# Optimization experiments

Hardware: AMD Instinct MI355X
Metric: run time of the kernel (lower is better)

The kernel has to match this reference:

```python
import math
import jax, jax.numpy as jnp
import numpy as np

D = 4  # BWGNN d


def calculate_theta2(d):
    # Faithful numeric reimplementation of the sympy version.
    # f_i(x) = (x/2)^i (1-x/2)^(d-i) / (2*Beta(i+1, d+1-i)); the original code
    # keeps only the d lowest-order (ascending) coefficients, dropping x^d.
    thetas = []
    for i in range(d):
        c1 = np.zeros(i + 1); c1[i] = 0.5 ** i                      # (x/2)^i
        c2 = np.array([math.comb(d - i, j) * (-0.5) ** j
                       for j in range(d - i + 1)])                   # (1-x/2)^(d-i)
        c = np.convolve(c1, c2)                                      # ascending, len d+1
        B = math.factorial(i) * math.factorial(d - i) / math.factorial(d + 1)
        c = c / (2.0 * B)
        thetas.append([float(c[j]) for j in range(d)])               # coeff[d-i] slicing
    return thetas

THETAS = calculate_theta2(D)


def setup_inputs() -> dict:
    key = jax.random.key(0)
    k1, k2, k3, k4 = jax.random.split(key, 4)
    N, E, F_in, H = 100000, 1600000, 128, 64
    feature = jax.random.normal(k1, (N, F_in), dtype=jnp.float32)
    edge_index = jax.random.randint(k2, (2, E), 0, N, dtype=jnp.int32)
    W = jax.random.normal(k3, (F_in, H), dtype=jnp.float32) * 0.05
    b = jax.random.normal(k4, (H,), dtype=jnp.float32) * 0.05
    return {"feature": feature, "edge_index": edge_index, "W": W, "b": b}


def reference(feature, edge_index, W, b):
    N = feature.shape[0]
    src, dst = edge_index[0], edge_index[1]
    # out_degrees: number of out-edges per node (src side), clamped to >= 1
    deg = jax.ops.segment_sum(jnp.ones_like(src, dtype=jnp.float32), src,
                              num_segments=N)
    D_invsqrt = jnp.maximum(deg, 1.0) ** -0.5  # [N]
    D_invsqrt = D_invsqrt[:, None]             # [N,1]

    h = jax.nn.leaky_relu(feature @ W + b, negative_slope=0.01)  # [N,H]

    def unn_laplacian(feat):
        # feat - D^{-1/2} A^T D^{-1/2} feat  (copy_u + sum over dst)
        msg = (feat * D_invsqrt)[src]                          # [E,H]
        agg = jax.ops.segment_sum(msg, dst, num_segments=N)    # [N,H]
        return feat - agg * D_invsqrt

    outs = []
    for theta in THETAS:
        feat = h
        acc = theta[0] * feat
        for k in range(1, len(theta)):
            feat = unn_laplacian(feat)
            acc = acc + theta[k] * feat
        outs.append(acc)
    return jnp.concatenate(outs, axis=1)  # [N, len(THETAS)*H]
```

## Files before the change

### kernel.cpp

```cpp
#include <hip/hip_runtime.h>

#define THREADS 256
#define T1 4096
#define BCAP 8192
#define NBMAX 512

__device__ __forceinline__ float bf2f(unsigned short u) {
    return __uint_as_float(((unsigned int)u) << 16);
}
__device__ __forceinline__ unsigned short f2bf(float x) {
    unsigned int u = __float_as_uint(x);
    u += 0x7fffu + ((u >> 16) & 1u);
    return (unsigned short)(u >> 16);
}

__global__ void zero_kernel(int* __restrict__ p, int n) {
    const int i = blockIdx.x * blockDim.x + threadIdx.x;
    if (i < n) p[i] = 0;
}

__global__ void bin_kernel(const int* __restrict__ key, const int* __restrict__ val,
                           int* __restrict__ gFill, unsigned int* __restrict__ gBuf, int E) {
    __shared__ int cnt[NBMAX], scanB[NBMAX], gbase[NBMAX], place[NBMAX];
    __shared__ unsigned int stage[T1];
    __shared__ unsigned int stageAddr[T1];
    const int tid = threadIdx.x;
    const int tileStart = blockIdx.x * T1;
    const int tileCnt = min(T1, E - tileStart);

    for (int i = tid; i < NBMAX; i += THREADS) { cnt[i] = 0; place[i] = 0; }
    __syncthreads();

    for (int i = tid; i < tileCnt; i += THREADS)
        atomicAdd(&cnt[key[tileStart + i] >> 8], 1);
    __syncthreads();

    if (tid < 64) {
        const int base = tid * 8;
        int loc[8]; int s = 0;
        #pragma unroll
        for (int k = 0; k < 8; ++k) { loc[k] = s; s += cnt[base + k]; }
        int run = s;
        #pragma unroll
        for (int off = 1; off < 64; off <<= 1) {
            int t = __shfl_up(run, off);
            if (tid >= off) run += t;
        }
        const int excl = run - s;
        #pragma unroll
        for (int k = 0; k < 8; ++k) scanB[base + k] = excl + loc[k];
    }
    __syncthreads();

    for (int i = tid; i < NBMAX; i += THREADS)
        gbase[i] = atomicAdd(&gFill[i], cnt[i]);
    __syncthreads();

    for (int i = tid; i < tileCnt; i += THREADS) {
        const int kk = key[tileStart + i];
        const int vv = val[tileStart + i];
        const int b = kk >> 8;
        const unsigned int rec = ((unsigned int)(kk & 255) << 17) | (unsigned int)vv;
        const int pos = atomicAdd(&place[b], 1);
        const int li = scanB[b] + pos;
        const int gi = gbase[b] + pos;
        stage[li] = rec;
        stageAddr[li] = (gi < BCAP) ? (unsigned int)(b * BCAP + gi) : 0xFFFFFFFFu;
    }
    __syncthreads();

    for (int i = tid; i < tileCnt; i += THREADS) {
        const unsigned int a = stageAddr[i];
        if (a != 0xFFFFFFFFu) gBuf[a] = stage[i];
    }
}

__global__ void scanb_kernel(const int* __restrict__ gFill, int* __restrict__ gBase,
                             int* __restrict__ rowptr, int nb, int N) {
    __shared__ int s[NBMAX];
    const int tid = threadIdx.x;
    const int v = (tid < nb) ? min(gFill[tid], BCAP) : 0;
    s[tid] = v;
    __syncthreads();
    for (int off = 1; off < NBMAX; off <<= 1) {
        int t = (tid >= off) ? s[tid - off] : 0;
        __syncthreads();
        s[tid] += t;
        __syncthreads();
    }
    if (tid < nb) gBase[tid] = s[tid] - v;
    if (tid == NBMAX - 1) rowptr[N] = s[NBMAX - 1];
}

__global__ void csr_kernel(const int* __restrict__ gFill, const int* __restrict__ gBase,
                           const unsigned int* __restrict__ gBuf,
                           int* __restrict__ rowptr, int* __restrict__ col, int N) {
    __shared__ int fillT[256], offT[256], place[256], sc[256];
    __shared__ int colT[BCAP];
    __shared__ int nwrite;
    const int tid = threadIdx.x;
    const int b = blockIdx.x;
    const int nrec = min(gFill[b], BCAP);
    const int base = gBase[b];

    fillT[tid] = 0; place[tid] = 0;
    __syncthreads();
    for (int i = tid; i < nrec; i += THREADS)
        atomicAdd(&fillT[gBuf[(size_t)b * BCAP + i] >> 17], 1);
    __syncthreads();

    int v = fillT[tid];
    sc[tid] = v;
    __syncthreads();
    for (int off = 1; off < 256; off <<= 1) {
        int t = (tid >= off) ? sc[tid - off] : 0;
        __syncthreads();
        sc[tid] += t;
        __syncthreads();
    }
    offT[tid] = sc[tid] - v;
    if (tid == 255) nwrite = sc[255];
    __syncthreads();

    const int node0 = b << 8;
    const int nvalid = min(256, N - node0);
    if (tid < nvalid) rowptr[node0 + tid] = base + offT[tid];

    for (int i = tid; i < nrec; i += THREADS) {
        const unsigned int rec = gBuf[(size_t)b * BCAP + i];
        const int dlow = rec >> 17;
        const int s = rec & 0x1FFFF;
        const int pos = atomicAdd(&place[dlow], 1);
        colT[offT[dlow] + pos] = s;
    }
    __syncthreads();

    const int nw = nwrite;
    for (int i = tid; i < nw; i += THREADS) col[base + i] = colT[i];
}

__global__ void deg_kernel2(const int* __restrict__ gFill, const unsigned int* __restrict__ gBuf,
                            int* __restrict__ deg, int N) {
    __shared__ int cntT[256];
    const int tid = threadIdx.x;
    const int b = blockIdx.x;
    const int nrec = min(gFill[b], BCAP);
    for (int i = tid; i < 256; i += THREADS) cntT[i] = 0;
    __syncthreads();
    for (int i = tid; i < nrec; i += THREADS)
        atomicAdd(&cntT[gBuf[(size_t)b * BCAP + i] >> 17], 1);
    __syncthreads();
    const int node0 = b << 8;
    const int nvalid = min(256, N - node0);
    for (int t = tid; t < nvalid; t += THREADS) deg[node0 + t] = cntT[t];
}

__global__ void count_fb(const int* __restrict__ src, const int* __restrict__ dst,
                         int* __restrict__ deg, int* __restrict__ cntd, int E) {
    const int stride = gridDim.x * blockDim.x;
    for (int i = blockIdx.x * blockDim.x + threadIdx.x; i < E; i += stride) {
        atomicAdd(&deg[src[i]], 1);
        atomicAdd(&cntd[dst[i]], 1);
    }
}
__global__ void scan_fb(const int* __restrict__ cnt, int* __restrict__ rowptr, int N) {
    __shared__ int s[256];
    __shared__ int carry;
    const int tid = threadIdx.x;
    if (tid == 0) carry = 0;
    __syncthreads();
    for (int basei = 0; basei < N; basei += 256) {
        const int i = basei + tid;
        const int v = (i < N) ? cnt[i] : 0;
        s[tid] = v;
        __syncthreads();
        for (int off = 1; off < 256; off <<= 1) {
            int t = (tid >= off) ? s[tid - off] : 0;
            __syncthreads();
            s[tid] += t;
            __syncthreads();
        }
        if (i < N) rowptr[i] = carry + s[tid] - v;
        __syncthreads();
        if (tid == 0) carry += s[255];
        __syncthreads();
    }
    if (tid == 0) rowptr[N] = carry;
}
__global__ void fill_fb(const int* __restrict__ src, const int* __restrict__ dst,
                        const int* __restrict__ rowptr, int* __restrict__ place,
                        int* __restrict__ col, int E) {
    const int stride = gridDim.x * blockDim.x;
    for (int i = blockIdx.x * blockDim.x + threadIdx.x; i < E; i += stride) {
        const int d = dst[i];
        col[rowptr[d] + atomicAdd(&place[d], 1)] = src[i];
    }
}

__global__ void gemm_leaky(const float* __restrict__ feat, const float* __restrict__ W,
                           const float* __restrict__ b, const int* __restrict__ deg,
                           float* __restrict__ out, int N) {
    __shared__ float Wl[128 * 64];
    __shared__ float fl[64][132];
    __shared__ float bl[64];

    {
        const float4* W4 = (const float4*)W;
        float4* Wl4 = (float4*)Wl;
        for (int i = threadIdx.x; i < 2048; i += THREADS) Wl4[i] = W4[i];
        if (threadIdx.x < 64) bl[threadIdx.x] = b[threadIdx.x];
    }

    const int cg = threadIdx.x & 15;
    const int rg = threadIdx.x >> 4;
    const int ntiles = (N + 63) >> 6;
    char* base = (char*)out;

    for (int tile = blockIdx.x; tile < ntiles; tile += gridDim.x) {
        const int n0 = tile << 6;
        __syncthreads();
        for (int i = threadIdx.x; i < 2048; i += THREADS) {
            int rr = i >> 5;
            int kk = i & 31;
            float4 v = make_float4(0.f, 0.f, 0.f, 0.f);
            if (n0 + rr < N) v = ((const float4*)(feat + (size_t)(n0 + rr) * 128))[kk];
            *((float4*)&fl[rr][kk * 4]) = v;
        }
        __syncthreads();

        float acc[4][4];
        #pragma unroll
        for (int j = 0; j < 4; ++j) {
            float bv = bl[cg * 4 + j];
            acc[0][j] = bv; acc[1][j] = bv; acc[2][j] = bv; acc[3][j] = bv;
        }

        #pragma unroll 4
        for (int k = 0; k < 128; ++k) {
            const float4 w = *((const float4*)&Wl[k * 64 + cg * 4]);
            const float f0 = fl[rg * 4 + 0][k];
            const float f1 = fl[rg * 4 + 1][k];
            const float f2 = fl[rg * 4 + 2][k];
            const float f3 = fl[rg * 4 + 3][k];
            acc[0][0] += f0 * w.x; acc[0][1] += f0 * w.y; acc[0][2] += f0 * w.z; acc[0][3] += f0 * w.w;
            acc[1][0] += f1 * w.x; acc[1][1] += f1 * w.y; acc[1][2] += f1 * w.z; acc[1][3] += f1 * w.w;
            acc[2][0] += f2 * w.x; acc[2][1] += f2 * w.y; acc[2][2] += f2 * w.z; acc[2][3] += f2 * w.w;
            acc[3][0] += f3 * w.x; acc[3][1] += f3 * w.y; acc[3][2] += f3 * w.z; acc[3][3] += f3 * w.w;
        }

        #pragma unroll
        for (int i = 0; i < 4; ++i) {
            const int n = n0 + rg * 4 + i;
            if (n < N) {
                const float dv = rsqrtf(fmaxf((float)deg[n], 1.0f));
                ushort4 o;
                float v0 = acc[i][0] > 0.f ? acc[i][0] : 0.01f * acc[i][0];
                float v1 = acc[i][1] > 0.f ? acc[i][1] : 0.01f * acc[i][1];
                float v2 = acc[i][2] > 0.f ? acc[i][2] : 0.01f * acc[i][2];
                float v3 = acc[i][3] > 0.f ? acc[i][3] : 0.01f * acc[i][3];
                o.x = f2bf(v0 * dv); o.y = f2bf(v1 * dv); o.z = f2bf(v2 * dv); o.w = f2bf(v3 * dv);
                *((ushort4*)(base + (size_t)n * 1024 + cg * 8)) = o;
            }
        }
    }
}

__global__ void hop_kernel(const int* __restrict__ rowptr, const int* __restrict__ col,
                           const int* __restrict__ deg, float* __restrict__ out,
                           int N, int prevOff, int nextOff) {
    const int lane = threadIdx.x & 63;
    const int nwaves = (gridDim.x * blockDim.x) >> 6;
    char* base = (char*)out;
    for (int n = (blockIdx.x * blockDim.x + threadIdx.x) >> 6; n < N; n += nwaves) {
        const int beg = rowptr[n];
        const int end = rowptr[n + 1];
        float acc = 0.0f;
        for (int e0 = beg; e0 < end; e0 += 64) {
            const int idx = e0 + lane;
            const int c = (idx < end) ? col[idx] : 0;
            const int m = min(64, end - e0);
            int j = 0;
            for (; j + 4 <= m; j += 4) {
                const int s0 = __shfl(c, j);
                const int s1 = __shfl(c, j + 1);
                const int s2 = __shfl(c, j + 2);
                const int s3 = __shfl(c, j + 3);
                const float v0 = bf2f(*(const unsigned short*)(base + (size_t)s0 * 1024 + prevOff + lane * 2));
                const float v1 = bf2f(*(const unsigned short*)(base + (size_t)s1 * 1024 + prevOff + lane * 2));
                const float v2 = bf2f(*(const unsigned short*)(base + (size_t)s2 * 1024 + prevOff + lane * 2));
                const float v3 = bf2f(*(const unsigned short*)(base + (size_t)s3 * 1024 + prevOff + lane * 2));
                acc += (v0 + v1) + (v2 + v3);
            }
            for (; j < m; ++j) {
                const int s = __shfl(c, j);
                acc += bf2f(*(const unsigned short*)(base + (size_t)s * 1024 + prevOff + lane * 2));
            }
        }
        const float own = bf2f(*(const unsigned short*)(base + (size_t)n * 1024 + prevOff + lane * 2));
        const float d = fmaxf((float)deg[n], 1.0f);
        const float sn = own - acc / d;
        *(unsigned short*)(base + (size_t)n * 1024 + nextOff + lane * 2) = f2bf(sn);
    }
}

__global__ void combine_kernel(float* __restrict__ out, const int* __restrict__ deg, int N) {
    const int lane = threadIdx.x & 63;
    const int nwaves = (gridDim.x * blockDim.x) >> 6;
    char* base = (char*)out;
    for (int n = (blockIdx.x * blockDim.x + threadIdx.x) >> 6; n < N; n += nwaves) {
        char* row = base + (size_t)n * 1024;
        const float s0 = bf2f(*(const unsigned short*)(row + 0   + lane * 2));
        const float s1 = bf2f(*(const unsigned short*)(row + 128 + lane * 2));
        const float s2 = bf2f(*(const unsigned short*)(row + 256 + lane * 2));
        const float s3 = bf2f(*(const unsigned short*)(row + 384 + lane * 2));
        const float sc = sqrtf(fmaxf((float)deg[n], 1.0f));
        const float h  = s0 * sc;
        const float p1 = s1 * sc;
        const float p2 = s2 * sc;
        const float p3 = s3 * sc;
        const float o0 = 2.5f * h - 5.0f * p1 + 3.75f * p2 - 1.25f * p3;
        const float o1 = 5.0f * p1 - 7.5f * p2 + 3.75f * p3;
        const float o2 = 3.75f * (p2 - p3);
        const float o3 = 1.25f * p3;
        float* frow = (float*)row;
        frow[lane]       = o0;
        frow[64 + lane]  = o1;
        frow[128 + lane] = o2;
        frow[192 + lane] = o3;
    }
}

extern "C" void kernel_launch(void* const* d_in, const int* in_sizes, int n_in,
                              void* d_out, int out_size, void* d_ws, size_t ws_size,
                              hipStream_t stream) {
    const float* feature = (const float*)d_in[0];
    const int*   eidx    = (const int*)d_in[1];
    const float* W       = (const float*)d_in[2];
    const float* b       = (const float*)d_in[3];
    float* out = (float*)d_out;

    const int N = in_sizes[0] / 128;
    const int E = in_sizes[1] / 2;
    const int* src = eidx;
    const int* dst = eidx + E;

    const int nb = (N + 255) >> 8;

    int* deg    = (int*)d_ws;
    int* fill   = deg + N;
    int* rowptr = fill + N;
    int* col    = rowptr + (N + 1);
    int* gFillD = col + E;
    int* gFillS = gFillD + NBMAX;
    int* gBase  = gFillS + NBMAX;
    unsigned int* gBufD = (unsigned int*)(gBase + NBMAX);
    unsigned int* gBufS = gBufD + (size_t)nb * BCAP;

    if (N <= 131072) {
        zero_kernel<<<(2 * NBMAX + THREADS - 1) / THREADS, THREADS, 0, stream>>>(gFillD, 2 * NBMAX);
        const int tiles = (E + T1 - 1) / T1;
        bin_kernel<<<tiles, THREADS, 0, stream>>>(dst, src, gFillD, gBufD, E);
        bin_kernel<<<tiles, THREADS, 0, stream>>>(src, src, gFillS, gBufS, E);
        scanb_kernel<<<1, NBMAX, 0, stream>>>(gFillD, gBase, rowptr, nb, N);
        csr_kernel<<<nb, THREADS, 0, stream>>>(gFillD, gBase, gBufD, rowptr, col, N);
        deg_kernel2<<<nb, THREADS, 0, stream>>>(gFillS, gBufS, deg, N);
    } else {
        zero_kernel<<<(2 * N + THREADS - 1) / THREADS, THREADS, 0, stream>>>(deg, 2 * N);
        count_fb<<<2048, THREADS, 0, stream>>>(src, dst, deg, fill, E);
        scan_fb<<<1, 256, 0, stream>>>(fill, rowptr, N);
        zero_kernel<<<(N + THREADS - 1) / THREADS, THREADS, 0, stream>>>(fill, N);
        fill_fb<<<2048, THREADS, 0, stream>>>(src, dst, rowptr, fill, col, E);
    }

    const int gemm_blocks = (N + 63) / 64;
    gemm_leaky<<<gemm_blocks, THREADS, 0, stream>>>(feature, W, b, deg, out, N);

    const int gblocks = (N + 3) / 4;
    hop_kernel<<<gblocks, THREADS, 0, stream>>>(rowptr, col, deg, out, N, 0, 128);
    hop_kernel<<<gblocks, THREADS, 0, stream>>>(rowptr, col, deg, out, N, 128, 256);
    hop_kernel<<<gblocks, THREADS, 0, stream>>>(rowptr, col, deg, out, N, 256, 384);

    combine_kernel<<<gblocks, THREADS, 0, stream>>>(out, deg, N);
}
```

Measured before the change: 288.4 us.

## Use compact bf16 hop buffers, fuse combine into last hop, merge binning passes

The per-hop bf16 states move out of the strided 1KB output rows into dense 128-byte-per-node workspace buffers. This improves cache-line use on the random neighbour gathers. The gather now has each 16-lane group load a ushort4 for a different edge, handling 4 edges per step, and reduces across groups with xor shuffles. The separate combine kernel is folded into the last hop, and the two edge-binning launches are merged into one kernel with a smaller tile so one edge read serves both. The cost is more workspace memory and extra shuffle reductions per node.

```diff
diff --git a/kernel.cpp b/kernel.cpp
--- a/kernel.cpp
+++ b/kernel.cpp
@@ -1,7 +1,7 @@
 #include <hip/hip_runtime.h>
 
 #define THREADS 256
-#define T1 4096
+#define T1 2048
 #define BCAP 8192
 #define NBMAX 512
 
@@ -19,24 +19,34 @@
     if (i < n) p[i] = 0;
 }
 
-__global__ void bin_kernel(const int* __restrict__ key, const int* __restrict__ val,
-                           int* __restrict__ gFill, unsigned int* __restrict__ gBuf, int E) {
-    __shared__ int cnt[NBMAX], scanB[NBMAX], gbase[NBMAX], place[NBMAX];
-    __shared__ unsigned int stage[T1];
-    __shared__ unsigned int stageAddr[T1];
+__global__ void bin2_kernel(const int* __restrict__ src, const int* __restrict__ dst,
+                            int* __restrict__ gFillD, unsigned int* __restrict__ gBufD,
+                            int* __restrict__ gFillS, unsigned int* __restrict__ gBufS, int E) {
+    __shared__ int cntD[NBMAX], scanD[NBMAX], gbaseD[NBMAX], placeD[NBMAX];
+    __shared__ int cntS[NBMAX], scanS[NBMAX], gbaseS[NBMAX], placeS[NBMAX];
+    __shared__ unsigned int stageD[T1], addrD[T1];
+    __shared__ unsigned int stageS[T1], addrS[T1];
     const int tid = threadIdx.x;
     const int tileStart = blockIdx.x * T1;
     const int tileCnt = min(T1, E - tileStart);
 
-    for (int i = tid; i < NBMAX; i += THREADS) { cnt[i] = 0; place[i] = 0; }
-    __syncthreads();
-
-    for (int i = tid; i < tileCnt; i += THREADS)
-        atomicAdd(&cnt[key[tileStart + i] >> 8], 1);
-    __syncthreads();
-
-    if (tid < 64) {
-        const int base = tid * 8;
+    for (int i = tid; i < NBMAX; i += THREADS) {
+        cntD[i] = 0; placeD[i] = 0; cntS[i] = 0; placeS[i] = 0;
+    }
+    __syncthreads();
+
+    for (int i = tid; i < tileCnt; i += THREADS) {
+        atomicAdd(&cntD[dst[tileStart + i] >> 8], 1);
+        atomicAdd(&cntS[src[tileStart + i] >> 8], 1);
+    }
+    __syncthreads();
+
+    if (tid < 128) {
+        const int w = tid >> 6;
+        const int l = tid & 63;
+        const int* cnt = w ? cntS : cntD;
+        int* sout = w ? scanS : scanD;
+        const int base = l * 8;
         int loc[8]; int s = 0;
         #pragma unroll
         for (int k = 0; k < 8; ++k) { loc[k] = s; s += cnt[base + k]; }
@@ -44,34 +54,48 @@
         #pragma unroll
         for (int off = 1; off < 64; off <<= 1) {
             int t = __shfl_up(run, off);
-            if (tid >= off) run += t;
+            if (l >= off) run += t;
         }
         const int excl = run - s;
         #pragma unroll
-        for (int k = 0; k < 8; ++k) scanB[base + k] = excl + loc[k];
-    }
-    __syncthreads();
-
-    for (int i = tid; i < NBMAX; i += THREADS)
-        gbase[i] = atomicAdd(&gFill[i], cnt[i]);
+        for (int k = 0; k < 8; ++k) sout[base + k] = excl + loc[k];
+    }
+    __syncthreads();
+
+    for (int i = tid; i < NBMAX; i += THREADS) {
+        gbaseD[i] = atomicAdd(&gFillD[i], cntD[i]);
+        gbaseS[i] = atomicAdd(&gFillS[i], cntS[i]);
+    }
     __syncthreads();
 
     for (int i = tid; i < tileCnt; i += THREADS) {
-        const int kk = key[tileStart + i];
-        const int vv = val[tileStart + i];
-        const int b = kk >> 8;
-        const unsigned int rec = ((unsigned int)(kk & 255) << 17) | (unsigned int)vv;
-        const int pos = atomicAdd(&place[b], 1);
-        const int li = scanB[b] + pos;
-        const int gi = gbase[b] + pos;
-        stage[li] = rec;
-        stageAddr[li] = (gi < BCAP) ? (unsigned int)(b * BCAP + gi) : 0xFFFFFFFFu;
+        const int ss = src[tileStart + i];
+        const int dd = dst[tileStart + i];
+        {
+            const int b = dd >> 8;
+            const unsigned int rec = ((unsigned int)(dd & 255) << 17) | (unsigned int)ss;
+            const int pos = atomicAdd(&placeD[b], 1);
+            const int li = scanD[b] + pos;
+            const int gi = gbaseD[b] + pos;
+            stageD[li] = rec;
+            addrD[li] = (gi < BCAP) ? (unsigned int)(b * BCAP + gi) : 0xFFFFFFFFu;
+        }
+        {
+            const int b = ss >> 8;
+            const int pos = atomicAdd(&placeS[b], 1);
+            const int li = scanS[b] + pos;
+            const int gi = gbaseS[b] + pos;
+            stageS[li] = (unsigned int)(ss & 255);
+            addrS[li] = (gi < BCAP) ? (unsigned int)(b * BCAP + gi) : 0xFFFFFFFFu;
+        }
     }
     __syncthreads();
 
     for (int i = tid; i < tileCnt; i += THREADS) {
-        const unsigned int a = stageAddr[i];
-        if (a != 0xFFFFFFFFu) gBuf[a] = stage[i];
+        const unsigned int aD = addrD[i];
+        if (aD != 0xFFFFFFFFu) gBufD[aD] = stageD[i];
+        const unsigned int aS = addrS[i];
+        if (aS != 0xFFFFFFFFu) gBufS[aS] = stageS[i];
     }
 }
 
@@ -148,7 +172,7 @@
     for (int i = tid; i < 256; i += THREADS) cntT[i] = 0;
     __syncthreads();
     for (int i = tid; i < nrec; i += THREADS)
-        atomicAdd(&cntT[gBuf[(size_t)b * BCAP + i] >> 17], 1);
+        atomicAdd(&cntT[gBuf[(size_t)b * BCAP + i] & 255], 1);
     __syncthreads();
     const int node0 = b << 8;
     const int nvalid = min(256, N - node0);
@@ -199,7 +223,7 @@
 
 __global__ void gemm_leaky(const float* __restrict__ feat, const float* __restrict__ W,
                            const float* __restrict__ b, const int* __restrict__ deg,
-                           float* __restrict__ out, int N) {
+                           unsigned short* __restrict__ S0, int N) {
     __shared__ float Wl[128 * 64];
     __shared__ float fl[64][132];
     __shared__ float bl[64];
@@ -214,7 +238,6 @@
     const int cg = threadIdx.x & 15;
     const int rg = threadIdx.x >> 4;
     const int ntiles = (N + 63) >> 6;
-    char* base = (char*)out;
 
     for (int tile = blockIdx.x; tile < ntiles; tile += gridDim.x) {
         const int n0 = tile << 6;
@@ -259,74 +282,85 @@
                 float v2 = acc[i][2] > 0.f ? acc[i][2] : 0.01f * acc[i][2];
                 float v3 = acc[i][3] > 0.f ? acc[i][3] : 0.01f * acc[i][3];
                 o.x = f2bf(v0 * dv); o.y = f2bf(v1 * dv); o.z = f2bf(v2 * dv); o.w = f2bf(v3 * dv);
-                *((ushort4*)(base + (size_t)n * 1024 + cg * 8)) = o;
+                *((ushort4*)(S0 + (size_t)n * 64 + cg * 4)) = o;
             }
         }
     }
 }
 
+template<bool FINAL>
 __global__ void hop_kernel(const int* __restrict__ rowptr, const int* __restrict__ col,
-                           const int* __restrict__ deg, float* __restrict__ out,
-                           int N, int prevOff, int nextOff) {
+                           const int* __restrict__ deg,
+                           const unsigned short* __restrict__ Sprev,
+                           unsigned short* __restrict__ Snext,
+                           const unsigned short* __restrict__ S0,
+                           const unsigned short* __restrict__ S1,
+                           float* __restrict__ out, int N) {
     const int lane = threadIdx.x & 63;
+    const int g  = lane >> 4;
+    const int cl = lane & 15;
     const int nwaves = (gridDim.x * blockDim.x) >> 6;
-    char* base = (char*)out;
     for (int n = (blockIdx.x * blockDim.x + threadIdx.x) >> 6; n < N; n += nwaves) {
         const int beg = rowptr[n];
         const int end = rowptr[n + 1];
-        float acc = 0.0f;
+        float ax = 0.f, ay = 0.f, az = 0.f, aw = 0.f;
         for (int e0 = beg; e0 < end; e0 += 64) {
             const int idx = e0 + lane;
             const int c = (idx < end) ? col[idx] : 0;
             const int m = min(64, end - e0);
-            int j = 0;
-            for (; j + 4 <= m; j += 4) {
-                const int s0 = __shfl(c, j);
-                const int s1 = __shfl(c, j + 1);
-                const int s2 = __shfl(c, j + 2);
-                const int s3 = __shfl(c, j + 3);
-                const float v0 = bf2f(*(const unsigned short*)(base + (size_t)s0 * 1024 + prevOff + lane * 2));
-                const float v1 = bf2f(*(const unsigned short*)(base + (size_t)s1 * 1024 + prevOff + lane * 2));
-                const float v2 = bf2f(*(const unsigned short*)(base + (size_t)s2 * 1024 + prevOff + lane * 2));
-                const float v3 = bf2f(*(const unsigned short*)(base + (size_t)s3 * 1024 + prevOff + lane * 2));
-                acc += (v0 + v1) + (v2 + v3);
+            for (int j = 0; j < m; j += 4) {
+                const int jg = j + g;
+                const int s = __shfl(c, jg & 63);
+                if (jg < m) {
+                    const ushort4 u = *(const ushort4*)(Sprev + (size_t)s * 64 + cl * 4);
+                    ax += bf2f(u.x); ay += bf2f(u.y); az += bf2f(u.z); aw += bf2f(u.w);
+                }
             }
-            for (; j < m; ++j) {
-                const int s = __shfl(c, j);
-                acc += bf2f(*(const unsigned short*)(base + (size_t)s * 1024 + prevOff + lane * 2));
+        }
+        ax += __shfl_xor(ax, 16); ay += __shfl_xor(ay, 16); az += __shfl_xor(az, 16); aw += __shfl_xor(aw, 16);
+        ax += __shfl_xor(ax, 32); ay += __shfl_xor(ay, 32); az += __shfl_xor(az, 32); aw += __shfl_xor(aw, 32);
+
+        const float d = fmaxf((float)deg[n], 1.0f);
+        const float inv = 1.0f / d;
+        const ushort4 ow = *(const ushort4*)(Sprev + (size_t)n * 64 + cl * 4);
+        const float snx = bf2f(ow.x) - ax * inv;
+        const float sny = bf2f(ow.y) - ay * inv;
+        const float snz = bf2f(ow.z) - az * inv;
+        const float snw = bf2f(ow.w) - aw * inv;
+
+        if (!FINAL) {
+            if (g == 0) {
+                ushort4 o;
+                o.x = f2bf(snx); o.y = f2bf(sny); o.z = f2bf(snz); o.w = f2bf(snw);
+                *((ushort4*)(Snext + (size_t)n * 64 + cl * 4)) = o;
             }
-        }
-        const float own = bf2f(*(const unsigned short*)(base + (size_t)n * 1024 + prevOff + lane * 2));
-        const float d = fmaxf((float)deg[n], 1.0f);
-        const float sn = own - acc / d;
-        *(unsigned short*)(base + (size_t)n * 1024 + nextOff + lane * 2) = f2bf(sn);
-    }
-}
-
-__global__ void combine_kernel(float* __restrict__ out, const int* __restrict__ deg, int N) {
-    const int lane = threadIdx.x & 63;
-    const int nwaves = (gridDim.x * blockDim.x) >> 6;
-    char* base = (char*)out;
-    for (int n = (blockIdx.x * blockDim.x + threadIdx.x) >> 6; n < N; n += nwaves) {
-        char* row = base + (size_t)n * 1024;
-        const float s0 = bf2f(*(const unsigned short*)(row + 0   + lane * 2));
-        const float s1 = bf2f(*(const unsigned short*)(row + 128 + lane * 2));
-        const float s2 = bf2f(*(const unsigned short*)(row + 256 + lane * 2));
-        const float s3 = bf2f(*(const unsigned short*)(row + 384 + lane * 2));
-        const float sc = sqrtf(fmaxf((float)deg[n], 1.0f));
-        const float h  = s0 * sc;
-        const float p1 = s1 * sc;
-        const float p2 = s2 * sc;
-        const float p3 = s3 * sc;
-        const float o0 = 2.5f * h - 5.0f * p1 + 3.75f * p2 - 1.25f * p3;
-        const float o1 = 5.0f * p1 - 7.5f * p2 + 3.75f * p3;
-        const float o2 = 3.75f * (p2 - p3);
-        const float o3 = 1.25f * p3;
-        float* frow = (float*)row;
-        frow[lane]       = o0;
-        frow[64 + lane]  = o1;
-        frow[128 + lane] = o2;
-        frow[192 + lane] = o3;
+        } else {
+            const float sc = sqrtf(d);
+            const ushort4 u0 = *(const ushort4*)(S0 + (size_t)n * 64 + cl * 4);
+            const ushort4 u1 = *(const ushort4*)(S1 + (size_t)n * 64 + cl * 4);
+            const float hx = bf2f(u0.x) * sc, hy = bf2f(u0.y) * sc, hz = bf2f(u0.z) * sc, hw = bf2f(u0.w) * sc;
+            const float p1x = bf2f(u1.x) * sc, p1y = bf2f(u1.y) * sc, p1z = bf2f(u1.z) * sc, p1w = bf2f(u1.w) * sc;
+            const float p2x = bf2f(ow.x) * sc, p2y = bf2f(ow.y) * sc, p2z = bf2f(ow.z) * sc, p2w = bf2f(ow.w) * sc;
+            const float p3x = snx * sc, p3y = sny * sc, p3z = snz * sc, p3w = snw * sc;
+            float4 o;
+            if (g == 0) {
+                o.x = 2.5f*hx - 5.0f*p1x + 3.75f*p2x - 1.25f*p3x;
+                o.y = 2.5f*hy - 5.0f*p1y + 3.75f*p2y - 1.25f*p3y;
+                o.z = 2.5f*hz - 5.0f*p1z + 3.75f*p2z - 1.25f*p3z;
+                o.w = 2.5f*hw - 5.0f*p1w + 3.75f*p2w - 1.25f*p3w;
+            } else if (g == 1) {
+                o.x = 5.0f*p1x - 7.5f*p2x + 3.75f*p3x;
+                o.y = 5.0f*p1y - 7.5f*p2y + 3.75f*p3y;
+                o.z = 5.0f*p1z - 7.5f*p2z + 3.75f*p3z;
+                o.w = 5.0f*p1w - 7.5f*p2w + 3.75f*p3w;
+            } else if (g == 2) {
+                o.x = 3.75f*(p2x - p3x); o.y = 3.75f*(p2y - p3y);
+                o.z = 3.75f*(p2z - p3z); o.w = 3.75f*(p2w - p3w);
+            } else {
+                o.x = 1.25f*p3x; o.y = 1.25f*p3y; o.z = 1.25f*p3z; o.w = 1.25f*p3w;
+            }
+            *((float4*)(out + (size_t)n * 256 + g * 64 + cl * 4)) = o;
+        }
     }
 }
 
@@ -355,12 +389,14 @@
     int* gBase  = gFillS + NBMAX;
     unsigned int* gBufD = (unsigned int*)(gBase + NBMAX);
     unsigned int* gBufS = gBufD + (size_t)nb * BCAP;
+    unsigned short* S0 = (unsigned short*)(gBufS + (size_t)nb * BCAP);
+    unsigned short* S1 = S0 + (size_t)N * 64;
+    unsigned short* S2 = S1 + (size_t)N * 64;
 
     if (N <= 131072) {
         zero_kernel<<<(2 * NBMAX + THREADS - 1) / THREADS, THREADS, 0, stream>>>(gFillD, 2 * NBMAX);
         const int tiles = (E + T1 - 1) / T1;
-        bin_kernel<<<tiles, THREADS, 0, stream>>>(dst, src, gFillD, gBufD, E);
-        bin_kernel<<<tiles, THREADS, 0, stream>>>(src, src, gFillS, gBufS, E);
+        bin2_kernel<<<tiles, THREADS, 0, stream>>>(src, dst, gFillD, gBufD, gFillS, gBufS, E);
         scanb_kernel<<<1, NBMAX, 0, stream>>>(gFillD, gBase, rowptr, nb, N);
         csr_kernel<<<nb, THREADS, 0, stream>>>(gFillD, gBase, gBufD, rowptr, col, N);
         deg_kernel2<<<nb, THREADS, 0, stream>>>(gFillS, gBufS, deg, N);
@@ -373,12 +409,10 @@
     }
 
     const int gemm_blocks = (N + 63) / 64;
-    gemm_leaky<<<gemm_blocks, THREADS, 0, stream>>>(feature, W, b, deg, out, N);
+    gemm_leaky<<<gemm_blocks, THREADS, 0, stream>>>(feature, W, b, deg, S0, N);
 
     const int gblocks = (N + 3) / 4;
-    hop_kernel<<<gblocks, THREADS, 0, stream>>>(rowptr, col, deg, out, N, 0, 128);
-    hop_kernel<<<gblocks, THREADS, 0, stream>>>(rowptr, col, deg, out, N, 128, 256);
-    hop_kernel<<<gblocks, THREADS, 0, stream>>>(rowptr, col, deg, out, N, 256, 384);
-
-    combine_kernel<<<gblocks, THREADS, 0, stream>>>(out, deg, N);
-}
+    hop_kernel<false><<<gblocks, THREADS, 0, stream>>>(rowptr, col, deg, S0, S1, S0, S0, out, N);
+    hop_kernel<false><<<gblocks, THREADS, 0, stream>>>(rowptr, col, deg, S1, S2, S0, S0, out, N);
+    hop_kernel<true ><<<gblocks, THREADS, 0, stream>>>(rowptr, col, deg, S2, S2, S0, S1, out, N);
+}
```

Result: slower. 318.8 us (+10.5%).

## Store hop states in compact bf16 buffers, gather 8 edges per wave, fuse combine

Applied to the files above, without the earlier changes.

Hop states now live in separate dense bf16 arrays of 128 bytes per row instead of strided slices of the 1024-byte output rows. Each wave gathers eight neighbor rows at once using 16-byte loads per lane, then reduces across lane groups with xor shuffles. The final hop writes the polynomial combination straight to the output, which removes the separate combine kernel. The two binning launches are merged into one grid, and the degree records shrink to the low node bits. The aim is fewer scattered narrow loads and less cache-line waste in the gather, at the cost of extra workspace and a cross-lane reduction per node.

```diff
diff --git a/kernel.cpp b/kernel.cpp
--- a/kernel.cpp
+++ b/kernel.cpp
@@ -13,19 +13,27 @@
     u += 0x7fffu + ((u >> 16) & 1u);
     return (unsigned short)(u >> 16);
 }
+__device__ __forceinline__ float blo(unsigned int x) { return __uint_as_float(x << 16); }
+__device__ __forceinline__ float bhi(unsigned int x) { return __uint_as_float(x & 0xffff0000u); }
 
 __global__ void zero_kernel(int* __restrict__ p, int n) {
     const int i = blockIdx.x * blockDim.x + threadIdx.x;
     if (i < n) p[i] = 0;
 }
 
-__global__ void bin_kernel(const int* __restrict__ key, const int* __restrict__ val,
-                           int* __restrict__ gFill, unsigned int* __restrict__ gBuf, int E) {
+__global__ void bin_kernel(const int* __restrict__ src, const int* __restrict__ dst,
+                           int* __restrict__ gFillD, unsigned int* __restrict__ gBufD,
+                           int* __restrict__ gFillS, unsigned int* __restrict__ gBufS,
+                           int E, int tiles) {
     __shared__ int cnt[NBMAX], scanB[NBMAX], gbase[NBMAX], place[NBMAX];
-    __shared__ unsigned int stage[T1];
-    __shared__ unsigned int stageAddr[T1];
+    __shared__ unsigned int stage[T1], addr[T1];
     const int tid = threadIdx.x;
-    const int tileStart = blockIdx.x * T1;
+    const bool isS = blockIdx.x >= tiles;
+    const int tile = isS ? blockIdx.x - tiles : blockIdx.x;
+    const int* key = isS ? src : dst;
+    int* gFill = isS ? gFillS : gFillD;
+    unsigned int* gBuf = isS ? gBufS : gBufD;
+    const int tileStart = tile * T1;
     const int tileCnt = min(T1, E - tileStart);
 
     for (int i = tid; i < NBMAX; i += THREADS) { cnt[i] = 0; place[i] = 0; }
@@ -58,19 +66,19 @@
 
     for (int i = tid; i < tileCnt; i += THREADS) {
         const int kk = key[tileStart + i];
-        const int vv = val[tileStart + i];
         const int b = kk >> 8;
-        const unsigned int rec = ((unsigned int)(kk & 255) << 17) | (unsigned int)vv;
+        const unsigned int rec = isS ? (unsigned int)(kk & 255)
+                                     : (((unsigned int)(kk & 255) << 17) | (unsigned int)src[tileStart + i]);
         const int pos = atomicAdd(&place[b], 1);
         const int li = scanB[b] + pos;
         const int gi = gbase[b] + pos;
         stage[li] = rec;
-        stageAddr[li] = (gi < BCAP) ? (unsigned int)(b * BCAP + gi) : 0xFFFFFFFFu;
+        addr[li] = (gi < BCAP) ? (unsigned int)(b * BCAP + gi) : 0xFFFFFFFFu;
     }
     __syncthreads();
 
     for (int i = tid; i < tileCnt; i += THREADS) {
-        const unsigned int a = stageAddr[i];
+        const unsigned int a = addr[i];
         if (a != 0xFFFFFFFFu) gBuf[a] = stage[i];
     }
 }
@@ -148,7 +156,7 @@
     for (int i = tid; i < 256; i += THREADS) cntT[i] = 0;
     __syncthreads();
     for (int i = tid; i < nrec; i += THREADS)
-        atomicAdd(&cntT[gBuf[(size_t)b * BCAP + i] >> 17], 1);
+        atomicAdd(&cntT[gBuf[(size_t)b * BCAP + i] & 255], 1);
     __syncthreads();
     const int node0 = b << 8;
     const int nvalid = min(256, N - node0);
@@ -199,7 +207,7 @@
 
 __global__ void gemm_leaky(const float* __restrict__ feat, const float* __restrict__ W,
                            const float* __restrict__ b, const int* __restrict__ deg,
-                           float* __restrict__ out, int N) {
+                           unsigned short* __restrict__ S0, int N) {
     __shared__ float Wl[128 * 64];
     __shared__ float fl[64][132];
     __shared__ float bl[64];
@@ -214,7 +222,6 @@
     const int cg = threadIdx.x & 15;
     const int rg = threadIdx.x >> 4;
     const int ntiles = (N + 63) >> 6;
-    char* base = (char*)out;
 
     for (int tile = blockIdx.x; tile < ntiles; tile += gridDim.x) {
         const int n0 = tile << 6;
@@ -259,74 +266,96 @@
                 float v2 = acc[i][2] > 0.f ? acc[i][2] : 0.01f * acc[i][2];
                 float v3 = acc[i][3] > 0.f ? acc[i][3] : 0.01f * acc[i][3];
                 o.x = f2bf(v0 * dv); o.y = f2bf(v1 * dv); o.z = f2bf(v2 * dv); o.w = f2bf(v3 * dv);
-                *((ushort4*)(base + (size_t)n * 1024 + cg * 8)) = o;
+                *((ushort4*)(S0 + (size_t)n * 64 + cg * 4)) = o;
             }
         }
     }
 }
 
+template<bool FINAL>
 __global__ void hop_kernel(const int* __restrict__ rowptr, const int* __restrict__ col,
-                           const int* __restrict__ deg, float* __restrict__ out,
-                           int N, int prevOff, int nextOff) {
+                           const int* __restrict__ deg,
+                           const unsigned short* __restrict__ Sprev,
+                           unsigned short* __restrict__ Snext,
+                           const unsigned short* __restrict__ S0,
+                           const unsigned short* __restrict__ S1,
+                           float* __restrict__ out, int N) {
     const int lane = threadIdx.x & 63;
+    const int g = lane >> 3;
+    const int q = lane & 7;
     const int nwaves = (gridDim.x * blockDim.x) >> 6;
-    char* base = (char*)out;
     for (int n = (blockIdx.x * blockDim.x + threadIdx.x) >> 6; n < N; n += nwaves) {
         const int beg = rowptr[n];
         const int end = rowptr[n + 1];
-        float acc = 0.0f;
+        float a[8];
+        #pragma unroll
+        for (int k = 0; k < 8; ++k) a[k] = 0.f;
+
         for (int e0 = beg; e0 < end; e0 += 64) {
             const int idx = e0 + lane;
             const int c = (idx < end) ? col[idx] : 0;
             const int m = min(64, end - e0);
-            int j = 0;
-            for (; j + 4 <= m; j += 4) {
-                const int s0 = __shfl(c, j);
-                const int s1 = __shfl(c, j + 1);
-                const int s2 = __shfl(c, j + 2);
-                const int s3 = __shfl(c, j + 3);
-                const float v0 = bf2f(*(const unsigned short*)(base + (size_t)s0 * 1024 + prevOff + lane * 2));
-                const float v1 = bf2f(*(const unsigned short*)(base + (size_t)s1 * 1024 + prevOff + lane * 2));
-                const float v2 = bf2f(*(const unsigned short*)(base + (size_t)s2 * 1024 + prevOff + lane * 2));
-                const float v3 = bf2f(*(const unsigned short*)(base + (size_t)s3 * 1024 + prevOff + lane * 2));
-                acc += (v0 + v1) + (v2 + v3);
+            for (int j = 0; j < m; j += 8) {
+                const int jg = j + g;
+                const int s = __shfl(c, jg & 63);
+                if (jg < m) {
+                    const uint4 u = *(const uint4*)(Sprev + (size_t)s * 64 + q * 8);
+                    a[0] += blo(u.x); a[1] += bhi(u.x);
+                    a[2] += blo(u.y); a[3] += bhi(u.y);
+                    a[4] += blo(u.z); a[5] += bhi(u.z);
+                    a[6] += blo(u.w); a[7] += bhi(u.w);
+                }
             }
-            for (; j < m; ++j) {
-                const int s = __shfl(c, j);
-                acc += bf2f(*(const unsigned short*)(base + (size_t)s * 1024 + prevOff + lane * 2));
+        }
+        #pragma unroll
+        for (int k = 0; k < 8; ++k) {
+            a[k] += __shfl_xor(a[k], 8);
+            a[k] += __shfl_xor(a[k], 16);
+            a[k] += __shfl_xor(a[k], 32);
+        }
+
+        const float d = fmaxf((float)deg[n], 1.0f);
+        const float inv = 1.0f / d;
+        const uint4 uo = *(const uint4*)(Sprev + (size_t)n * 64 + q * 8);
+        float own[8], sn[8];
+        own[0] = blo(uo.x); own[1] = bhi(uo.x); own[2] = blo(uo.y); own[3] = bhi(uo.y);
+        own[4] = blo(uo.z); own[5] = bhi(uo.z); own[6] = blo(uo.w); own[7] = bhi(uo.w);
+        #pragma unroll
+        for (int k = 0; k < 8; ++k) sn[k] = own[k] - a[k] * inv;
+
+        if (!FINAL) {
+            if (g == 0) {
+                uint4 w;
+                w.x = (unsigned int)f2bf(sn[0]) | ((unsigned int)f2bf(sn[1]) << 16);
+                w.y = (unsigned int)f2bf(sn[2]) | ((unsigned int)f2bf(sn[3]) << 16);
+                w.z = (unsigned int)f2bf(sn[4]) | ((unsigned int)f2bf(sn[5]) << 16);
+                w.w = (unsigned int)f2bf(sn[6]) | ((unsigned int)f2bf(sn[7]) << 16);
+                *((uint4*)(Snext + (size_t)n * 64 + q * 8)) = w;
             }
-        }
-        const float own = bf2f(*(const unsigned short*)(base + (size_t)n * 1024 + prevOff + lane * 2));
-        const float d = fmaxf((float)deg[n], 1.0f);
-        const float sn = own - acc / d;
-        *(unsigned short*)(base + (size_t)n * 1024 + nextOff + lane * 2) = f2bf(sn);
-    }
-}
-
-__global__ void combine_kernel(float* __restrict__ out, const int* __restrict__ deg, int N) {
-    const int lane = threadIdx.x & 63;
-    const int nwaves = (gridDim.x * blockDim.x) >> 6;
-    char* base = (char*)out;
-    for (int n = (blockIdx.x * blockDim.x + threadIdx.x) >> 6; n < N; n += nwaves) {
-        char* row = base + (size_t)n * 1024;
-        const float s0 = bf2f(*(const unsigned short*)(row + 0   + lane * 2));
-        const float s1 = bf2f(*(const unsigned short*)(row + 128 + lane * 2));
-        const float s2 = bf2f(*(const unsigned short*)(row + 256 + lane * 2));
-        const float s3 = bf2f(*(const unsigned short*)(row + 384 + lane * 2));
-        const float sc = sqrtf(fmaxf((float)deg[n], 1.0f));
-        const float h  = s0 * sc;
-        const float p1 = s1 * sc;
-        const float p2 = s2 * sc;
-        const float p3 = s3 * sc;
-        const float o0 = 2.5f * h - 5.0f * p1 + 3.75f * p2 - 1.25f * p3;
-        const float o1 = 5.0f * p1 - 7.5f * p2 + 3.75f * p3;
-        const float o2 = 3.75f * (p2 - p3);
-        const float o3 = 1.25f * p3;
-        float* frow = (float*)row;
-        frow[lane]       = o0;
-        frow[64 + lane]  = o1;
-        frow[128 + lane] = o2;
-        frow[192 + lane] = o3;
+        } else if (g < 4) {
+            const float sc = sqrtf(d);
+            const uint4 u0 = *(const uint4*)(S0 + (size_t)n * 64 + q * 8);
+            const uint4 u1 = *(const uint4*)(S1 + (size_t)n * 64 + q * 8);
+            float h[8], p1[8];
+            h[0] = blo(u0.x); h[1] = bhi(u0.x); h[2] = blo(u0.y); h[3] = bhi(u0.y);
+            h[4] = blo(u0.z); h[5] = bhi(u0.z); h[6] = blo(u0.w); h[7] = bhi(u0.w);
+            p1[0] = blo(u1.x); p1[1] = bhi(u1.x); p1[2] = blo(u1.y); p1[3] = bhi(u1.y);
+            p1[4] = blo(u1.z); p1[5] = bhi(u1.z); p1[6] = blo(u1.w); p1[7] = bhi(u1.w);
+            float c0, c1, c2, c3;
+            if (g == 0)      { c0 = 2.5f; c1 = -5.0f; c2 = 3.75f;  c3 = -1.25f; }
+            else if (g == 1) { c0 = 0.f;  c1 = 5.0f;  c2 = -7.5f;  c3 = 3.75f;  }
+            else if (g == 2) { c0 = 0.f;  c1 = 0.f;   c2 = 3.75f;  c3 = -3.75f; }
+            else             { c0 = 0.f;  c1 = 0.f;   c2 = 0.f;    c3 = 1.25f;  }
+            float o[8];
+            #pragma unroll
+            for (int k = 0; k < 8; ++k) {
+                const float hv = h[k] * sc, p1v = p1[k] * sc, p2v = own[k] * sc, p3v = sn[k] * sc;
+                o[k] = c0 * hv + c1 * p1v + c2 * p2v + c3 * p3v;
+            }
+            float* op = out + (size_t)n * 256 + g * 64 + q * 8;
+            *((float4*)op)       = make_float4(o[0], o[1], o[2], o[3]);
+            *((float4*)(op + 4)) = make_float4(o[4], o[5], o[6], o[7]);
+        }
     }
 }
 
@@ -355,12 +384,14 @@
     int* gBase  = gFillS + NBMAX;
     unsigned int* gBufD = (unsigned int*)(gBase + NBMAX);
     unsigned int* gBufS = gBufD + (size_t)nb * BCAP;
+    unsigned short* S0 = (unsigned short*)(((uintptr_t)(gBufS + (size_t)nb * BCAP) + 255) & ~(uintptr_t)255);
+    unsigned short* S1 = S0 + (size_t)N * 64;
+    unsigned short* S2 = S1 + (size_t)N * 64;
 
     if (N <= 131072) {
         zero_kernel<<<(2 * NBMAX + THREADS - 1) / THREADS, THREADS, 0, stream>>>(gFillD, 2 * NBMAX);
         const int tiles = (E + T1 - 1) / T1;
-        bin_kernel<<<tiles, THREADS, 0, stream>>>(dst, src, gFillD, gBufD, E);
-        bin_kernel<<<tiles, THREADS, 0, stream>>>(src, src, gFillS, gBufS, E);
+        bin_kernel<<<2 * tiles, THREADS, 0, stream>>>(src, dst, gFillD, gBufD, gFillS, gBufS, E, tiles);
         scanb_kernel<<<1, NBMAX, 0, stream>>>(gFillD, gBase, rowptr, nb, N);
         csr_kernel<<<nb, THREADS, 0, stream>>>(gFillD, gBase, gBufD, rowptr, col, N);
         deg_kernel2<<<nb, THREADS, 0, stream>>>(gFillS, gBufS, deg, N);
@@ -373,12 +404,10 @@
     }
 
     const int gemm_blocks = (N + 63) / 64;
-    gemm_leaky<<<gemm_blocks, THREADS, 0, stream>>>(feature, W, b, deg, out, N);
+    gemm_leaky<<<gemm_blocks, THREADS, 0, stream>>>(feature, W, b, deg, S0, N);
 
     const int gblocks = (N + 3) / 4;
-    hop_kernel<<<gblocks, THREADS, 0, stream>>>(rowptr, col, deg, out, N, 0, 128);
-    hop_kernel<<<gblocks, THREADS, 0, stream>>>(rowptr, col, deg, out, N, 128, 256);
-    hop_kernel<<<gblocks, THREADS, 0, stream>>>(rowptr, col, deg, out, N, 256, 384);
-
-    combine_kernel<<<gblocks, THREADS, 0, stream>>>(out, deg, N);
-}
+    hop_kernel<false><<<gblocks, THREADS, 0, stream>>>(rowptr, col, deg, S0, S1, S0, S0, out, N);
+    hop_kernel<false><<<gblocks, THREADS, 0, stream>>>(rowptr, col, deg, S1, S2, S0, S0, out, N);
+    hop_kernel<true ><<<gblocks, THREADS, 0, stream>>>(rowptr, col, deg, S2, S2, S0, S1, out, N);
+}
```

After: 244.7 us. 15.1% less time.
